# Optimization experiments

Hardware: AMD Instinct MI355X
Metric: run time of the kernel (lower is better)

Reference implementation:

```python
import jax, jax.numpy as jnp
import numpy as np

EMB = 128
N_LEFT = 100000
N_RIGHT = 100000
N_EDGES = 600000
EDGE_FEAT = 1


def _ortho(key, shape):
    a = jax.random.normal(key, shape, dtype=jnp.float32)
    q, r = jnp.linalg.qr(a if shape[0] >= shape[1] else a.T)
    q = q * jnp.sign(jnp.diag(r))
    return q if shape[0] >= shape[1] else q.T


def setup_inputs() -> dict:
    key = jax.random.key(0)
    ks = jax.random.split(key, 12)
    return {
        "left_features": jax.random.normal(ks[0], (N_LEFT, EMB), dtype=jnp.float32),
        "edge_indices": jax.random.randint(ks[1], (2, N_EDGES), 0, N_LEFT, dtype=jnp.int32).astype(jnp.int64),
        "edge_features": jax.random.normal(ks[2], (N_EDGES, EDGE_FEAT), dtype=jnp.float32),
        "right_features": jax.random.normal(ks[3], (N_RIGHT, EMB), dtype=jnp.float32),
        "scatter_out_size": N_RIGHT,
        # parameters (orthogonal weights, zero biases, unit PreNorm scales)
        "W_left": _ortho(ks[4], (EMB, EMB)),
        "b_left": jnp.zeros((EMB,), jnp.float32),
        "W_edge": _ortho(ks[5], (EMB, EDGE_FEAT)),
        "W_right": _ortho(ks[6], (EMB, EMB)),
        "scale_final": jnp.ones((1,), jnp.float32),
        "W_final": _ortho(ks[7], (EMB, EMB)),
        "b_final": jnp.zeros((EMB,), jnp.float32),
        "scale_post": jnp.ones((1,), jnp.float32),
        "W_out1": _ortho(ks[8], (EMB, 2 * EMB)),
        "b_out1": jnp.zeros((EMB,), jnp.float32),
        "W_out2": _ortho(ks[9], (EMB, EMB)),
        "b_out2": jnp.zeros((EMB,), jnp.float32),
    }


def reference(left_features, edge_indices, edge_features, right_features,
              scatter_out_size, W_left, b_left, W_edge, W_right,
              scale_final, W_final, b_final, scale_post,
              W_out1, b_out1, W_out2, b_out2):
    # node / edge projections
    left_proj = left_features @ W_left.T + b_left            # [n_left, emb]
    edge_proj = edge_features @ W_edge.T                     # [n_edges, emb]
    right_proj = right_features @ W_right.T                  # [n_right, emb]
    # gather per-edge messages and combine
    joint = left_proj[edge_indices[0]] + edge_proj + right_proj[edge_indices[1]]
    # feature_module_final: PreNorm(scale only) -> ReLU -> Linear
    joint = jax.nn.relu(joint * scale_final) @ W_final.T + b_final
    # scatter-add onto right-side nodes (right_to_left=False)
    conv = jax.ops.segment_sum(joint, edge_indices[1], num_segments=scatter_out_size)
    conv = conv * scale_post
    # output MLP on [conv ; prev_right]
    h = jnp.concatenate([conv, right_features], axis=1)      # [n_right, 2*emb]
    h = jax.nn.relu(h @ W_out1.T + b_out1)
    return h @ W_out2.T + b_out2
```

## Files before the change

### kernel.cpp

```cpp
#include <hip/hip_runtime.h>

#define EMB 128

typedef __attribute__((ext_vector_type(8))) short short8;
typedef __attribute__((ext_vector_type(4))) float floatx4;

#define MFMA(a, b, c) __builtin_amdgcn_mfma_f32_16x16x32_bf16((a), (b), (c), 0, 0, 0)

__device__ __forceinline__ ushort f2b(float f) {
    unsigned u = __float_as_uint(f);
    return (ushort)((u + 0x7fff + ((u >> 16) & 1)) >> 16);
}
__device__ __forceinline__ float b2f(ushort h) {
    return __uint_as_float(((unsigned)h) << 16);
}
__device__ __forceinline__ short8 cvt8(const float* p) {
    float4 f0 = *(const float4*)p;
    float4 f1 = *(const float4*)(p + 4);
    short8 v;
    v[0] = f2b(f0.x); v[1] = f2b(f0.y); v[2] = f2b(f0.z); v[3] = f2b(f0.w);
    v[4] = f2b(f1.x); v[5] = f2b(f1.y); v[6] = f2b(f1.z); v[7] = f2b(f1.w);
    return v;
}

__global__ void k_cvt_all(const float* __restrict__ w0, const float* __restrict__ w1,
                          const float* __restrict__ w2, const float* __restrict__ w3,
                          const float* __restrict__ w4, ushort* __restrict__ dst) {
    int i = blockIdx.x * blockDim.x + threadIdx.x;
    const float* src; int off;
    if (i < 16384)      { src = w0; off = i; }
    else if (i < 32768) { src = w1; off = i - 16384; }
    else if (i < 49152) { src = w2; off = i - 32768; }
    else if (i < 81920) { src = w3; off = i - 49152; }
    else                { src = w4; off = i - 81920; }
    dst[i] = f2b(src[off]);
}

__global__ __launch_bounds__(256) void k_proj_mfma(const float* __restrict__ XL,
                                                   const float* __restrict__ XR,
                                                   const ushort* __restrict__ WLb,
                                                   const ushort* __restrict__ WRb,
                                                   const float* __restrict__ bias,
                                                   ushort* __restrict__ YL,
                                                   ushort* __restrict__ YR,
                                                   int n, int nblk) {
    int bid = blockIdx.x;
    const float* X; const ushort* Wb; ushort* Y; int has_bias;
    if (bid < nblk) { X = XL; Wb = WLb; Y = YL; has_bias = 1; }
    else            { X = XR; Wb = WRb; Y = YR; has_bias = 0; bid -= nblk; }

    int t = threadIdx.x, wave = t >> 6, lane = t & 63;
    int m = lane & 15, quad = lane >> 4;
    int rp = (wave & 1) * 32, colg = (wave >> 1) * 64;
    size_t row0 = (size_t)bid * 64;

    short8 a[2][4];
#pragma unroll
    for (int rt = 0; rt < 2; rt++) {
        size_t row = row0 + rp + rt * 16 + m;
        if (row > (size_t)(n - 1)) row = (size_t)(n - 1);
        const float* xr = X + row * EMB;
#pragma unroll
        for (int ks = 0; ks < 4; ks++)
            a[rt][ks] = cvt8(xr + ks * 32 + quad * 8);
    }
#pragma unroll
    for (int ct = 0; ct < 4; ct++) {
        int col = colg + ct * 16 + m;
        floatx4 acc0 = {0.f, 0.f, 0.f, 0.f}, acc1 = {0.f, 0.f, 0.f, 0.f};
#pragma unroll
        for (int ks = 0; ks < 4; ks++) {
            short8 b = *(const short8*)(Wb + (size_t)col * EMB + ks * 32 + quad * 8);
            acc0 = MFMA(a[0][ks], b, acc0);
            acc1 = MFMA(a[1][ks], b, acc1);
        }
        float bb = has_bias ? bias[col] : 0.f;
        size_t r0 = row0 + rp + quad * 4;
#pragma unroll
        for (int r = 0; r < 4; r++) {
            size_t row = r0 + r;
            if (row < (size_t)n) Y[row * EMB + col] = f2b(acc0[r] + bb);
            row += 16;
            if (row < (size_t)n) Y[row * EMB + col] = f2b(acc1[r] + bb);
        }
    }
}

__global__ void k_hist(const int* __restrict__ eidx, int* __restrict__ cnt,
                       int n_edges) {
    int e = blockIdx.x * blockDim.x + threadIdx.x;
    if (e < n_edges) atomicAdd(&cnt[eidx[n_edges + e]], 1);
}

#define SCAN_CHUNK 4096
__global__ __launch_bounds__(1024) void k_scan1(const int* __restrict__ cnt,
                                                int* __restrict__ offs,
                                                int* __restrict__ bsum, int n) {
    __shared__ int buf[1024];
    int t = threadIdx.x;
    int i0 = blockIdx.x * SCAN_CHUNK + t * 4;
    int v[4];
#pragma unroll
    for (int u = 0; u < 4; u++) { int i = i0 + u; v[u] = (i < n) ? cnt[i] : 0; }
    int s = v[0] + v[1] + v[2] + v[3];
    buf[t] = s;
    __syncthreads();
    for (int d = 1; d < 1024; d <<= 1) {
        int x = (t >= d) ? buf[t - d] : 0;
        __syncthreads();
        buf[t] += x;
        __syncthreads();
    }
    int excl = buf[t] - s;
#pragma unroll
    for (int u = 0; u < 4; u++) { int i = i0 + u; if (i < n) offs[i] = excl; excl += v[u]; }
    if (t == 1023) bsum[blockIdx.x] = buf[1023];
}

__global__ __launch_bounds__(1024) void k_scan2(const int* __restrict__ bsum,
                                                int* __restrict__ offs,
                                                int* __restrict__ cursor, int n) {
    int bid = blockIdx.x;
    int base = 0;
    for (int j = 0; j < bid; j++) base += bsum[j];
    int i0 = bid * SCAN_CHUNK + threadIdx.x * 4;
#pragma unroll
    for (int u = 0; u < 4; u++) {
        int i = i0 + u;
        if (i < n) { int o = offs[i] + base; offs[i] = o; cursor[i] = o; }
    }
}

__global__ void k_perm(const int* __restrict__ eidx, const float* __restrict__ ef,
                       int* __restrict__ cursor, int2* __restrict__ sle,
                       int n_edges) {
    int e = blockIdx.x * blockDim.x + threadIdx.x;
    if (e < n_edges) {
        int r = eidx[n_edges + e];
        int p = atomicAdd(&cursor[r], 1);
        int2 v; v.x = eidx[e]; v.y = __float_as_int(ef[e]);
        sle[p] = v;
    }
}

__global__ __launch_bounds__(256) void k_reduce(const ushort* __restrict__ Pl,
                                                const ushort* __restrict__ Pr,
                                                const int2* __restrict__ sle,
                                                const float* __restrict__ We,
                                                const int* __restrict__ offs,
                                                const float* __restrict__ scale_final,
                                                ushort* __restrict__ S,
                                                int n_right, int n_edges) {
    int r = blockIdx.x * 4 + (threadIdx.x >> 6);
    int lane = threadIdx.x & 63;
    float scale = scale_final[0];
    float2 we = *(const float2*)(We + lane * 2);
    ushort2 pru = *(const ushort2*)(Pr + (size_t)r * EMB + lane * 2);
    float prx = b2f(pru.x), pry = b2f(pru.y);
    float ax = 0.f, ay = 0.f;
    int s0 = offs[r];
    int s1 = (r + 1 < n_right) ? offs[r + 1] : n_edges;
    int ei = s0;
    for (; ei + 2 <= s1; ei += 2) {
        int2 e0 = sle[ei], e1 = sle[ei + 1];
        ushort2 p0 = *(const ushort2*)(Pl + (size_t)e0.x * EMB + lane * 2);
        ushort2 p1 = *(const ushort2*)(Pl + (size_t)e1.x * EMB + lane * 2);
        float f0 = __int_as_float(e0.y), f1 = __int_as_float(e1.y);
        ax += fmaxf((b2f(p0.x) + prx + f0 * we.x) * scale, 0.f);
        ay += fmaxf((b2f(p0.y) + pry + f0 * we.y) * scale, 0.f);
        ax += fmaxf((b2f(p1.x) + prx + f1 * we.x) * scale, 0.f);
        ay += fmaxf((b2f(p1.y) + pry + f1 * we.y) * scale, 0.f);
    }
    if (ei < s1) {
        int2 e0 = sle[ei];
        ushort2 p0 = *(const ushort2*)(Pl + (size_t)e0.x * EMB + lane * 2);
        float f0 = __int_as_float(e0.y);
        ax += fmaxf((b2f(p0.x) + prx + f0 * we.x) * scale, 0.f);
        ay += fmaxf((b2f(p0.y) + pry + f0 * we.y) * scale, 0.f);
    }
    ushort2 o; o.x = f2b(ax); o.y = f2b(ay);
    *(ushort2*)(S + (size_t)r * EMB + lane * 2) = o;
}

__global__ __launch_bounds__(256) void k_out_mfma(const ushort* __restrict__ S,
                                                  const float* __restrict__ right,
                                                  const ushort* __restrict__ Wfb,
                                                  const float* __restrict__ bf,
                                                  const int* __restrict__ deg,
                                                  const float* __restrict__ sc_post,
                                                  const ushort* __restrict__ W1b,
                                                  const float* __restrict__ b1,
                                                  const ushort* __restrict__ W2b,
                                                  const float* __restrict__ b2,
                                                  float* __restrict__ out, int n) {
    __shared__ ushort H[64][136];
    __shared__ ushort T[64][136];
    __shared__ float degs[64];
    int t = threadIdx.x, wave = t >> 6, lane = t & 63;
    int m = lane & 15, quad = lane >> 4;
    int rp = (wave & 1) * 32, colg = (wave >> 1) * 64;
    size_t row0 = (size_t)blockIdx.x * 64;
    float sp = sc_post[0];

    if (t < 64) {
        size_t rr = row0 + t;
        degs[t] = (rr < (size_t)n) ? (float)deg[rr] : 0.f;
    }

    short8 a1[2][4], ar[2][4];
#pragma unroll
    for (int rt = 0; rt < 2; rt++) {
        size_t row = row0 + rp + rt * 16 + m;
        if (row > (size_t)(n - 1)) row = (size_t)(n - 1);
        const ushort* sr = S + row * EMB;
        const float* rr = right + row * EMB;
#pragma unroll
        for (int ks = 0; ks < 4; ks++) {
            a1[rt][ks] = *(const short8*)(sr + ks * 32 + quad * 8);
            ar[rt][ks] = cvt8(rr + ks * 32 + quad * 8);
        }
    }
    __syncthreads();

#pragma unroll
    for (int ct = 0; ct < 4; ct++) {
        int col = colg + ct * 16 + m;
        floatx4 acc0 = {0.f, 0.f, 0.f, 0.f}, acc1 = {0.f, 0.f, 0.f, 0.f};
#pragma unroll
        for (int ks = 0; ks < 4; ks++) {
            short8 b = *(const short8*)(Wfb + (size_t)col * EMB + ks * 32 + quad * 8);
            acc0 = MFMA(a1[0][ks], b, acc0);
            acc1 = MFMA(a1[1][ks], b, acc1);
        }
        float bb = bf[col];
        int r0 = rp + quad * 4;
#pragma unroll
        for (int r = 0; r < 4; r++) {
            H[r0 + r][col]      = f2b((acc0[r] + degs[r0 + r] * bb) * sp);
            H[r0 + 16 + r][col] = f2b((acc1[r] + degs[r0 + 16 + r] * bb) * sp);
        }
    }
    __syncthreads();

    short8 a2[2][4];
#pragma unroll
    for (int rt = 0; rt < 2; rt++)
#pragma unroll
        for (int ks = 0; ks < 4; ks++)
            a2[rt][ks] = *(const short8*)(&H[rp + rt * 16 + m][ks * 32 + quad * 8]);
#pragma unroll
    for (int ct = 0; ct < 4; ct++) {
        int col = colg + ct * 16 + m;
        floatx4 acc0 = {0.f, 0.f, 0.f, 0.f}, acc1 = {0.f, 0.f, 0.f, 0.f};
        const ushort* wrow = W1b + (size_t)col * 256;
#pragma unroll
        for (int ks = 0; ks < 4; ks++) {
            short8 b = *(const short8*)(wrow + ks * 32 + quad * 8);
            acc0 = MFMA(a2[0][ks], b, acc0);
            acc1 = MFMA(a2[1][ks], b, acc1);
        }
#pragma unroll
        for (int ks = 0; ks < 4; ks++) {
            short8 b = *(const short8*)(wrow + 128 + ks * 32 + quad * 8);
            acc0 = MFMA(ar[0][ks], b, acc0);
            acc1 = MFMA(ar[1][ks], b, acc1);
        }
        float bb = b1[col];
        int r0 = rp + quad * 4;
#pragma unroll
        for (int r = 0; r < 4; r++) {
            T[r0 + r][col]      = f2b(fmaxf(acc0[r] + bb, 0.f));
            T[r0 + 16 + r][col] = f2b(fmaxf(acc1[r] + bb, 0.f));
        }
    }
    __syncthreads();

    short8 a3[2][4];
#pragma unroll
    for (int rt = 0; rt < 2; rt++)
#pragma unroll
        for (int ks = 0; ks < 4; ks++)
            a3[rt][ks] = *(const short8*)(&T[rp + rt * 16 + m][ks * 32 + quad * 8]);
#pragma unroll
    for (int ct = 0; ct < 4; ct++) {
        int col = colg + ct * 16 + m;
        floatx4 acc0 = {0.f, 0.f, 0.f, 0.f}, acc1 = {0.f, 0.f, 0.f, 0.f};
#pragma unroll
        for (int ks = 0; ks < 4; ks++) {
            short8 b = *(const short8*)(W2b + (size_t)col * EMB + ks * 32 + quad * 8);
            acc0 = MFMA(a3[0][ks], b, acc0);
            acc1 = MFMA(a3[1][ks], b, acc1);
        }
        float bb = b2[col];
        size_t r0 = row0 + rp + quad * 4;
#pragma unroll
        for (int r = 0; r < 4; r++) {
            size_t row = r0 + r;
            if (row < (size_t)n) out[row * EMB + col] = acc0[r] + bb;
            row += 16;
            if (row < (size_t)n) out[row * EMB + col] = acc1[r] + bb;
        }
    }
}

extern "C" void kernel_launch(void* const* d_in, const int* in_sizes, int n_in,
                              void* d_out, int out_size, void* d_ws, size_t ws_size,
                              hipStream_t stream) {
    const float* left   = (const float*)d_in[0];
    const int*   eidx   = (const int*)  d_in[1];
    const float* efeat  = (const float*)d_in[2];
    const float* right  = (const float*)d_in[3];
    const float* W_left = (const float*)d_in[5];
    const float* b_left = (const float*)d_in[6];
    const float* W_edge = (const float*)d_in[7];
    const float* W_right= (const float*)d_in[8];
    const float* sc_fin = (const float*)d_in[9];
    const float* W_fin  = (const float*)d_in[10];
    const float* b_fin  = (const float*)d_in[11];
    const float* sc_post= (const float*)d_in[12];
    const float* W_out1 = (const float*)d_in[13];
    const float* b_out1 = (const float*)d_in[14];
    const float* W_out2 = (const float*)d_in[15];
    const float* b_out2 = (const float*)d_in[16];

    int n_left  = in_sizes[0] / EMB;
    int n_edges = in_sizes[2];
    int n_right = in_sizes[3] / EMB;

    ushort* us = (ushort*)d_ws;
    ushort* Wl_b = us;
    ushort* Wr_b = us + 16384;
    ushort* Wf_b = us + 32768;
    ushort* W1_b = us + 49152;
    ushort* W2_b = us + 81920;
    ushort* Pl   = us + 98304;
    ushort* Pr   = Pl + (size_t)n_left * EMB;
    ushort* S    = Pr + (size_t)n_right * EMB;
    int* cnt    = (int*)(S + (size_t)n_right * EMB);
    int* offs   = cnt + n_right;
    int* cursor = offs + n_right;
    int* bsum   = cursor + n_right;
    int2* sle   = (int2*)(bsum + 64);

    hipMemsetAsync(cnt, 0, (size_t)n_right * sizeof(int), stream);

    k_cvt_all<<<384, 256, 0, stream>>>(W_left, W_right, W_fin, W_out1, W_out2, us);

    int eb = (n_edges + 255) / 256;
    k_hist<<<eb, 256, 0, stream>>>(eidx, cnt, n_edges);
    int nsb = (n_right + SCAN_CHUNK - 1) / SCAN_CHUNK;
    k_scan1<<<nsb, 1024, 0, stream>>>(cnt, offs, bsum, n_right);
    k_scan2<<<nsb, 1024, 0, stream>>>(bsum, offs, cursor, n_right);
    k_perm<<<eb, 256, 0, stream>>>(eidx, efeat, cursor, sle, n_edges);

    int nblk = (n_left + 63) / 64;
    k_proj_mfma<<<2 * nblk, 256, 0, stream>>>(left, right, Wl_b, Wr_b, b_left,
                                              Pl, Pr, n_left, nblk);

    k_reduce<<<n_right / 4, 256, 0, stream>>>(Pl, Pr, sle, W_edge, offs,
                                              sc_fin, S, n_right, n_edges);

    k_out_mfma<<<(n_right + 63) / 64, 256, 0, stream>>>(S, right, Wf_b, b_fin,
                                                        cnt, sc_post, W1_b, b_out1,
                                                        W2_b, b_out2,
                                                        (float*)d_out, n_right);
}
```

Baseline: 411.7 us.

## Merge independent kernels into combined launches, unroll reduce loop, reuse LDS buffer

Folds weight conversion and the edge histogram into one launch, and folds the edge permutation and the node projections into another, using block-index ranges to pick the work. This cuts launch count and lets independent work overlap inside a single grid. The reduce loop is unrolled to four edges per iteration to keep more gathers in flight. The output MLP reuses one shared-memory tile instead of two, which costs an extra barrier but lowers LDS use and may raise occupancy.

After: 404.8 us. No clear change (-1.7%).

```diff
diff --git a/kernel.cpp b/kernel.cpp
--- a/kernel.cpp
+++ b/kernel.cpp
@@ -23,73 +23,29 @@
     return v;
 }
 
-__global__ void k_cvt_all(const float* __restrict__ w0, const float* __restrict__ w1,
-                          const float* __restrict__ w2, const float* __restrict__ w3,
-                          const float* __restrict__ w4, ushort* __restrict__ dst) {
-    int i = blockIdx.x * blockDim.x + threadIdx.x;
-    const float* src; int off;
-    if (i < 16384)      { src = w0; off = i; }
-    else if (i < 32768) { src = w1; off = i - 16384; }
-    else if (i < 49152) { src = w2; off = i - 32768; }
-    else if (i < 81920) { src = w3; off = i - 49152; }
-    else                { src = w4; off = i - 81920; }
-    dst[i] = f2b(src[off]);
-}
-
-__global__ __launch_bounds__(256) void k_proj_mfma(const float* __restrict__ XL,
-                                                   const float* __restrict__ XR,
-                                                   const ushort* __restrict__ WLb,
-                                                   const ushort* __restrict__ WRb,
-                                                   const float* __restrict__ bias,
-                                                   ushort* __restrict__ YL,
-                                                   ushort* __restrict__ YR,
-                                                   int n, int nblk) {
+__global__ __launch_bounds__(256) void k_cvthist(const float* __restrict__ w0,
+                                                 const float* __restrict__ w1,
+                                                 const float* __restrict__ w2,
+                                                 const float* __restrict__ w3,
+                                                 const float* __restrict__ w4,
+                                                 ushort* __restrict__ dst,
+                                                 const int* __restrict__ eidx,
+                                                 int* __restrict__ cnt,
+                                                 int n_edges) {
     int bid = blockIdx.x;
-    const float* X; const ushort* Wb; ushort* Y; int has_bias;
-    if (bid < nblk) { X = XL; Wb = WLb; Y = YL; has_bias = 1; }
-    else            { X = XR; Wb = WRb; Y = YR; has_bias = 0; bid -= nblk; }
-
-    int t = threadIdx.x, wave = t >> 6, lane = t & 63;
-    int m = lane & 15, quad = lane >> 4;
-    int rp = (wave & 1) * 32, colg = (wave >> 1) * 64;
-    size_t row0 = (size_t)bid * 64;
-
-    short8 a[2][4];
-#pragma unroll
-    for (int rt = 0; rt < 2; rt++) {
-        size_t row = row0 + rp + rt * 16 + m;
-        if (row > (size_t)(n - 1)) row = (size_t)(n - 1);
-        const float* xr = X + row * EMB;
-#pragma unroll
-        for (int ks = 0; ks < 4; ks++)
-            a[rt][ks] = cvt8(xr + ks * 32 + quad * 8);
-    }
-#pragma unroll
-    for (int ct = 0; ct < 4; ct++) {
-        int col = colg + ct * 16 + m;
-        floatx4 acc0 = {0.f, 0.f, 0.f, 0.f}, acc1 = {0.f, 0.f, 0.f, 0.f};
-#pragma unroll
-        for (int ks = 0; ks < 4; ks++) {
-            short8 b = *(const short8*)(Wb + (size_t)col * EMB + ks * 32 + quad * 8);
-            acc0 = MFMA(a[0][ks], b, acc0);
-            acc1 = MFMA(a[1][ks], b, acc1);
-        }
-        float bb = has_bias ? bias[col] : 0.f;
-        size_t r0 = row0 + rp + quad * 4;
-#pragma unroll
-        for (int r = 0; r < 4; r++) {
-            size_t row = r0 + r;
-            if (row < (size_t)n) Y[row * EMB + col] = f2b(acc0[r] + bb);
-            row += 16;
-            if (row < (size_t)n) Y[row * EMB + col] = f2b(acc1[r] + bb);
-        }
-    }
-}
-
-__global__ void k_hist(const int* __restrict__ eidx, int* __restrict__ cnt,
-                       int n_edges) {
-    int e = blockIdx.x * blockDim.x + threadIdx.x;
-    if (e < n_edges) atomicAdd(&cnt[eidx[n_edges + e]], 1);
+    if (bid < 384) {
+        int i = bid * 256 + threadIdx.x;
+        const float* src; int off;
+        if (i < 16384)      { src = w0; off = i; }
+        else if (i < 32768) { src = w1; off = i - 16384; }
+        else if (i < 49152) { src = w2; off = i - 32768; }
+        else if (i < 81920) { src = w3; off = i - 49152; }
+        else                { src = w4; off = i - 81920; }
+        dst[i] = f2b(src[off]);
+    } else {
+        int e = (bid - 384) * 256 + threadIdx.x;
+        if (e < n_edges) atomicAdd(&cnt[eidx[n_edges + e]], 1);
+    }
 }
 
 #define SCAN_CHUNK 4096
@@ -131,15 +87,69 @@
     }
 }
 
-__global__ void k_perm(const int* __restrict__ eidx, const float* __restrict__ ef,
-                       int* __restrict__ cursor, int2* __restrict__ sle,
-                       int n_edges) {
-    int e = blockIdx.x * blockDim.x + threadIdx.x;
-    if (e < n_edges) {
-        int r = eidx[n_edges + e];
-        int p = atomicAdd(&cursor[r], 1);
-        int2 v; v.x = eidx[e]; v.y = __float_as_int(ef[e]);
-        sle[p] = v;
+__global__ __launch_bounds__(256) void k_permproj(const int* __restrict__ eidx,
+                                                  const float* __restrict__ ef,
+                                                  int* __restrict__ cursor,
+                                                  int2* __restrict__ sle,
+                                                  int n_edges,
+                                                  const float* __restrict__ XL,
+                                                  const float* __restrict__ XR,
+                                                  const ushort* __restrict__ WLb,
+                                                  const ushort* __restrict__ WRb,
+                                                  const float* __restrict__ bias,
+                                                  ushort* __restrict__ YL,
+                                                  ushort* __restrict__ YR,
+                                                  int n, int eb, int nblk) {
+    int bid = blockIdx.x;
+    if (bid < eb) {
+        int e = bid * 256 + threadIdx.x;
+        if (e < n_edges) {
+            int r = eidx[n_edges + e];
+            int p = atomicAdd(&cursor[r], 1);
+            int2 v; v.x = eidx[e]; v.y = __float_as_int(ef[e]);
+            sle[p] = v;
+        }
+        return;
+    }
+    bid -= eb;
+    const float* X; const ushort* Wb; ushort* Y; int has_bias;
+    if (bid < nblk) { X = XL; Wb = WLb; Y = YL; has_bias = 1; }
+    else            { X = XR; Wb = WRb; Y = YR; has_bias = 0; bid -= nblk; }
+
+    int t = threadIdx.x, wave = t >> 6, lane = t & 63;
+    int m = lane & 15, quad = lane >> 4;
+    int rp = (wave & 1) * 32, colg = (wave >> 1) * 64;
+    size_t row0 = (size_t)bid * 64;
+
+    short8 a[2][4];
+#pragma unroll
+    for (int rt = 0; rt < 2; rt++) {
+        size_t row = row0 + rp + rt * 16 + m;
+        if (row > (size_t)(n - 1)) row = (size_t)(n - 1);
+        const float* xr = X + row * EMB;
+#pragma unroll
+        for (int ks = 0; ks < 4; ks++)
+            a[rt][ks] = cvt8(xr + ks * 32 + quad * 8);
+    }
+#pragma unroll
+    for (int ct = 0; ct < 4; ct++) {
+        int col = colg + ct * 16 + m;
+        floatx4 acc0 = {0.f, 0.f, 0.f, 0.f}, acc1 = {0.f, 0.f, 0.f, 0.f};
+#pragma unroll
+        for (int ks = 0; ks < 4; ks++) {
+            short8 b = *(const short8*)(Wb + (size_t)col * EMB + ks * 32 + quad * 8);
+            acc0 = MFMA(a[0][ks], b, acc0);
+            acc1 = MFMA(a[1][ks], b, acc1);
+        }
+        float bb = has_bias ? bias[col] : 0.f;
+        size_t r0 = row0 + rp + quad * 4;
+#pragma unroll
+        for (int r = 0; r < 4; r++) {
+            size_t row = r0 + r;
+            if (row < (size_t)n) Y[row * EMB + col] = f2b(acc0[r] + bb);
+            row += 16;
+            if (row < (size_t)n) Y[row * EMB + col] = f2b(acc1[r] + bb);
+        }
     }
 }
 
@@ -161,17 +171,24 @@
     int s0 = offs[r];
     int s1 = (r + 1 < n_right) ? offs[r + 1] : n_edges;
     int ei = s0;
-    for (; ei + 2 <= s1; ei += 2) {
-        int2 e0 = sle[ei], e1 = sle[ei + 1];
+    for (; ei + 4 <= s1; ei += 4) {
+        int2 e0 = sle[ei], e1 = sle[ei + 1], e2 = sle[ei + 2], e3 = sle[ei + 3];
         ushort2 p0 = *(const ushort2*)(Pl + (size_t)e0.x * EMB + lane * 2);
         ushort2 p1 = *(const ushort2*)(Pl + (size_t)e1.x * EMB + lane * 2);
+        ushort2 p2 = *(const ushort2*)(Pl + (size_t)e2.x * EMB + lane * 2);
+        ushort2 p3 = *(const ushort2*)(Pl + (size_t)e3.x * EMB + lane * 2);
         float f0 = __int_as_float(e0.y), f1 = __int_as_float(e1.y);
+        float f2_ = __int_as_float(e2.y), f3 = __int_as_float(e3.y);
         ax += fmaxf((b2f(p0.x) + prx + f0 * we.x) * scale, 0.f);
         ay += fmaxf((b2f(p0.y) + pry + f0 * we.y) * scale, 0.f);
         ax += fmaxf((b2f(p1.x) + prx + f1 * we.x) * scale, 0.f);
         ay += fmaxf((b2f(p1.y) + pry + f1 * we.y) * scale, 0.f);
-    }
-    if (ei < s1) {
+        ax += fmaxf((b2f(p2.x) + prx + f2_ * we.x) * scale, 0.f);
+        ay += fmaxf((b2f(p2.y) + pry + f2_ * we.y) * scale, 0.f);
+        ax += fmaxf((b2f(p3.x) + prx + f3 * we.x) * scale, 0.f);
+        ay += fmaxf((b2f(p3.y) + pry + f3 * we.y) * scale, 0.f);
+    }
+    for (; ei < s1; ei++) {
         int2 e0 = sle[ei];
         ushort2 p0 = *(const ushort2*)(Pl + (size_t)e0.x * EMB + lane * 2);
         float f0 = __int_as_float(e0.y);
@@ -194,7 +211,6 @@
                                                   const float* __restrict__ b2,
                                                   float* __restrict__ out, int n) {
     __shared__ ushort H[64][136];
-    __shared__ ushort T[64][136];
     __shared__ float degs[64];
     int t = threadIdx.x, wave = t >> 6, lane = t & 63;
     int m = lane & 15, quad = lane >> 4;
@@ -248,6 +264,8 @@
 #pragma unroll
         for (int ks = 0; ks < 4; ks++)
             a2[rt][ks] = *(const short8*)(&H[rp + rt * 16 + m][ks * 32 + quad * 8]);
+    __syncthreads();
+
 #pragma unroll
     for (int ct = 0; ct < 4; ct++) {
         int col = colg + ct * 16 + m;
@@ -269,8 +287,8 @@
         int r0 = rp + quad * 4;
 #pragma unroll
         for (int r = 0; r < 4; r++) {
-            T[r0 + r][col]      = f2b(fmaxf(acc0[r] + bb, 0.f));
-            T[r0 + 16 + r][col] = f2b(fmaxf(acc1[r] + bb, 0.f));
+            H[r0 + r][col]      = f2b(fmaxf(acc0[r] + bb, 0.f));
+            H[r0 + 16 + r][col] = f2b(fmaxf(acc1[r] + bb, 0.f));
         }
     }
     __syncthreads();
@@ -280,7 +298,7 @@
     for (int rt = 0; rt < 2; rt++)
 #pragma unroll
         for (int ks = 0; ks < 4; ks++)
-            a3[rt][ks] = *(const short8*)(&T[rp + rt * 16 + m][ks * 32 + quad * 8]);
+            a3[rt][ks] = *(const short8*)(&H[rp + rt * 16 + m][ks * 32 + quad * 8]);
 #pragma unroll
     for (int ct = 0; ct < 4; ct++) {
         int col = colg + ct * 16 + m;
@@ -344,18 +362,20 @@
 
     hipMemsetAsync(cnt, 0, (size_t)n_right * sizeof(int), stream);
 
-    k_cvt_all<<<384, 256, 0, stream>>>(W_left, W_right, W_fin, W_out1, W_out2, us);
-
     int eb = (n_edges + 255) / 256;
-    k_hist<<<eb, 256, 0, stream>>>(eidx, cnt, n_edges);
+    int nblk = (n_left + 63) / 64;
+
+    k_cvthist<<<384 + eb, 256, 0, stream>>>(W_left, W_right, W_fin, W_out1,
+                                            W_out2, us, eidx, cnt, n_edges);
+
     int nsb = (n_right + SCAN_CHUNK - 1) / SCAN_CHUNK;
     k_scan1<<<nsb, 1024, 0, stream>>>(cnt, offs, bsum, n_right);
     k_scan2<<<nsb, 1024, 0, stream>>>(bsum, offs, cursor, n_right);
-    k_perm<<<eb, 256, 0, stream>>>(eidx, efeat, cursor, sle, n_edges);
-
-    int nblk = (n_left + 63) / 64;
-    k_proj_mfma<<<2 * nblk, 256, 0, stream>>>(left, right, Wl_b, Wr_b, b_left,
-                                              Pl, Pr, n_left, nblk);
+
+    k_permproj<<<eb + 2 * nblk, 256, 0, stream>>>(eidx, efeat, cursor, sle,
+                                                  n_edges, left, right,
+                                                  Wl_b, Wr_b, b_left,
+                                                  Pl, Pr, n_left, eb, nblk);
 
     k_reduce<<<n_right / 4, 256, 0, stream>>>(Pl, Pr, sle, W_edge, offs,
                                               sc_fin, S, n_right, n_edges);
```
